# Optimization experiments

Measured on AMD Instinct MI355X. Metric: run time of the kernel, lower is better.

## Reference

```python
import jax, jax.numpy as jnp
import numpy as np

DIM = 512
NUM_HEADS = 16
HEAD_DIM = DIM // NUM_HEADS
RES = (32, 32)
SEQ_SCALE = float(np.log(RES[0] * RES[1]))  # seq_length_scale buffer
TABLE = (2 * RES[0] - 1) * (2 * RES[1] - 1)  # 3969
EPS = 1e-12


def setup_inputs() -> dict:
    key = jax.random.key(0)
    ks = jax.random.split(key, 12)
    B, N, C = 8, RES[0] * RES[1], DIM
    s = 0.02
    return {
        "x": jax.random.normal(ks[0], (B, N, C), dtype=jnp.float32),
        "_h": RES[0],
        "_w": RES[1],
        "relative_pos_index": jax.random.randint(ks[1], (N, N), 0, TABLE, dtype=jnp.int32),
        "relative_coords_table": jax.random.uniform(ks[2], (TABLE, 2), dtype=jnp.float32, minval=-1.0, maxval=1.0),
        "qkv_w": jax.random.normal(ks[3], (3 * C, C), dtype=jnp.float32) * s,
        "qkv_b": jnp.zeros((3 * C,), dtype=jnp.float32),
        "proj_w": jax.random.normal(ks[4], (C, C), dtype=jnp.float32) * s,
        "proj_b": jnp.zeros((C,), dtype=jnp.float32),
        "temperature": jnp.full((NUM_HEADS, 1, 1), float(np.log(np.expm1(1.0 / 0.24))), dtype=jnp.float32),
        "query_embedding": jax.random.normal(ks[5], (NUM_HEADS, 1, HEAD_DIM), dtype=jnp.float32) * s,
        "cpb_fc1_w": jax.random.normal(ks[6], (512, 2), dtype=jnp.float32) * s,
        "cpb_fc1_b": jnp.zeros((512,), dtype=jnp.float32),
        "cpb_fc2_w": jax.random.normal(ks[7], (NUM_HEADS, 512), dtype=jnp.float32) * s,
        "cpb_fc2_b": jnp.zeros((NUM_HEADS,), dtype=jnp.float32),
    }


def _l2norm(t):
    # F.normalize(t, dim=-1): x / max(||x||, eps)
    n = jnp.sqrt(jnp.sum(t * t, axis=-1, keepdims=True))
    return t / jnp.maximum(n, EPS)


def reference(x, _h, _w, relative_pos_index, relative_coords_table,
              qkv_w, qkv_b, proj_w, proj_b, temperature, query_embedding,
              cpb_fc1_w, cpb_fc1_b, cpb_fc2_w, cpb_fc2_b):
    B, N, C = x.shape
    H, hd = NUM_HEADS, HEAD_DIM
    # qkv projection -> [B, N, 3H, hd] -> [B, 3H, N, hd]
    qkv = (x @ qkv_w.T + qkv_b).reshape(B, N, 3 * H, hd).transpose(0, 2, 1, 3)
    q, k, v = jnp.split(qkv, 3, axis=1)  # each [B, H, N, hd]
    # CPB MLP relative bias: [T,2] -> [T,H] -> gather -> [H,N,N]
    t = jax.nn.relu(relative_coords_table @ cpb_fc1_w.T + cpb_fc1_b) @ cpb_fc2_w.T + cpb_fc2_b
    rel_bias = t[relative_pos_index].transpose(2, 0, 1)  # [H, N, N]
    # cosine attention with learned softplus temperature and query embedding
    scale = jax.nn.softplus(temperature) * SEQ_SCALE  # [H,1,1]
    qn = (_l2norm(q) + query_embedding[None]) * scale[None]
    kn = _l2norm(k)
    attn = jnp.einsum('bhnd,bhmd->bhnm', qn, kn) + rel_bias[None]
    attn = jax.nn.softmax(attn, axis=-1)
    out = jnp.einsum('bhnm,bhmd->bhnd', attn, v)  # [B,H,N,hd]
    out = out.transpose(0, 2, 1, 3).reshape(B, N, C)
    return out @ proj_w.T + proj_b
```

## Files before the change

kernel.cpp:

```cpp
#include <hip/hip_runtime.h>
#include <cstdint>
#include <cstddef>

typedef _Float16 f16;
typedef _Float16 f16x4 __attribute__((ext_vector_type(4)));
typedef _Float16 f16x8 __attribute__((ext_vector_type(8)));
typedef float f32x4 __attribute__((ext_vector_type(4)));

#define MFMA32(a,b,c) __builtin_amdgcn_mfma_f32_16x16x32_f16((a),(b),(c),0,0,0)
#define MFMA16(a,b,c) __builtin_amdgcn_mfma_f32_16x16x16f16((a),(b),(c),0,0,0)

__device__ __forceinline__ float fexp2(float x) {
#if __has_builtin(__builtin_amdgcn_exp2f)
  return __builtin_amdgcn_exp2f(x);
#else
  return __expf(x * 0.69314718055994531f);
#endif
}

__device__ __forceinline__ void gload_lds16(const f16* g, f16* l) {
  __builtin_amdgcn_global_load_lds(
      (const __attribute__((address_space(1))) unsigned int*)g,
      (__attribute__((address_space(3))) unsigned int*)l, 16, 0, 0);
}

static constexpr size_t OFF_TCPB = 0;
static constexpr size_t OFF_BIAS = 262144;
static constexpr size_t OFF_XHI  = OFF_BIAS + 33554432;
static constexpr size_t OFF_XLO  = OFF_XHI + 8388608;
static constexpr size_t OFF_WHI  = OFF_XLO + 8388608;
static constexpr size_t OFF_WLO  = OFF_WHI + 1572864;
static constexpr size_t OFF_PW   = OFF_WLO + 1572864;
static constexpr size_t OFF_QHI  = OFF_PW  + 524288;
static constexpr size_t OFF_QLO  = OFF_QHI + 8388608;
static constexpr size_t OFF_KHI  = OFF_QLO + 8388608;
static constexpr size_t OFF_KLO  = OFF_KHI + 8388608;
static constexpr size_t OFF_VT   = OFF_KLO + 8388608;
static constexpr size_t OFF_AO   = OFF_VT  + 8388608;

__global__ __launch_bounds__(256) void k_convert(
    const float* __restrict__ x, const float* __restrict__ qw, const float* __restrict__ pwf,
    f16* __restrict__ xhi, f16* __restrict__ xlo,
    f16* __restrict__ whi, f16* __restrict__ wlo, f16* __restrict__ pw)
{
  int i = blockIdx.x * 256 + threadIdx.x;
  const float4* src; f16* dh; f16* dl; int j;
  if (i < 1048576)      { j = i;           src = (const float4*)x;   dh = xhi; dl = xlo; }
  else if (i < 1245184) { j = i - 1048576; src = (const float4*)qw;  dh = whi; dl = wlo; }
  else                  { j = i - 1245184; src = (const float4*)pwf; dh = pw;  dl = nullptr; }
  float4 v = src[j];
  f16x4 h;
  h[0] = (f16)v.x; h[1] = (f16)v.y; h[2] = (f16)v.z; h[3] = (f16)v.w;
  ((f16x4*)dh)[j] = h;
  if (dl) {
    f16x4 l;
    l[0] = (f16)(v.x - (float)h[0]); l[1] = (f16)(v.y - (float)h[1]);
    l[2] = (f16)(v.z - (float)h[2]); l[3] = (f16)(v.w - (float)h[3]);
    ((f16x4*)dl)[j] = l;
  }
}

__global__ __launch_bounds__(256) void k_cpb(
    const float* __restrict__ table, const float* __restrict__ w1, const float* __restrict__ b1,
    const float* __restrict__ w2, const float* __restrict__ b2, float* __restrict__ t_out)
{
  const int r = blockIdx.x * 4 + (threadIdx.x >> 6);
  const int lane = threadIdx.x & 63;
  if (r >= 3969) return;
  const float c0 = table[2*r], c1 = table[2*r+1];
  const int j0 = lane * 8;
  float h[8];
#pragma unroll
  for (int jj = 0; jj < 8; jj++) {
    int j = j0 + jj;
    float v = c0 * w1[2*j] + c1 * w1[2*j+1] + b1[j];
    h[jj] = v > 0.0f ? v : 0.0f;
  }
  float acc[16];
#pragma unroll
  for (int o = 0; o < 16; o++) {
    const float4* wp = (const float4*)(w2 + o*512 + j0);
    float4 a = wp[0], bb = wp[1];
    acc[o] = a.x*h[0] + a.y*h[1] + a.z*h[2] + a.w*h[3]
           + bb.x*h[4] + bb.y*h[5] + bb.z*h[6] + bb.w*h[7];
  }
#pragma unroll
  for (int o = 0; o < 16; o++) {
    float v = acc[o];
    for (int s = 1; s < 64; s <<= 1) v += __shfl_xor(v, s, 64);
    acc[o] = v;
  }
  if (lane == 0) {
#pragma unroll
    for (int o = 0; o < 16; o++)
      t_out[r*16 + o] = (acc[o] + b2[o]) * 1.4426950408889634f;
  }
}

__global__ __launch_bounds__(256) void k_bias(
    const int* __restrict__ idx, const float* __restrict__ t_cpb, f16* __restrict__ bias_t)
{
  const int m4 = blockIdx.x >> 6, ng = blockIdx.x & 63;
  const int h = threadIdx.x >> 4, nl = threadIdx.x & 15;
  const int n = ng*16 + nl;
  int4 I = *(const int4*)(idx + (size_t)n*1024 + m4*4);
  f16x4 o;
  o[0] = (f16)t_cpb[I.x*16 + h];
  o[1] = (f16)t_cpb[I.y*16 + h];
  o[2] = (f16)t_cpb[I.z*16 + h];
  o[3] = (f16)t_cpb[I.w*16 + h];
  *(f16x4*)(bias_t + (((size_t)h*256 + m4)*1024 + n)*4) = o;
}

__global__ __launch_bounds__(256) void k_qkv(
    const f16* __restrict__ xhi, const f16* __restrict__ xlo,
    const f16* __restrict__ whi, const f16* __restrict__ wlo,
    const float* __restrict__ qkvb, const float* __restrict__ temp, const float* __restrict__ qe,
    f16* __restrict__ qh_o, f16* __restrict__ kh_o, f16* __restrict__ vt_o)
{
  __shared__ __align__(16) f16 Ah[8][64][8];
  __shared__ __align__(16) f16 Al[8][64][8];
  __shared__ __align__(16) f16 Bh[8][64][8];
  __shared__ __align__(16) f16 Bl[8][64][8];
  const int tid = threadIdx.x, lane = tid & 63, w = tid >> 6;
  const int rsel = lane & 15, ksel = lane >> 4;
  const int bx = blockIdx.x & 63, by = blockIdx.x >> 6;
  const int m0 = bx << 7, n0 = by << 7;
  const bool SPLIT = (by < 8);

  const size_t aoff = (size_t)(m0 + w*32 + rsel)*512 + ksel*8;
  const size_t boff = (size_t)(n0 + w*32 + rsel)*512 + ksel*8;
  const f16 *gA0 = xhi + aoff,  *gA1 = gA0 + 16*512;
  const f16 *gAl0 = xlo + aoff, *gAl1 = gAl0 + 16*512;
  const f16 *gB0 = whi + boff,  *gB1 = gB0 + 16*512;
  const f16 *gBl0 = wlo + boff, *gBl1 = gBl0 + 16*512;
  f16 *lA0 = &Ah[2*w][0][0],  *lA1 = &Ah[2*w+1][0][0];
  f16 *lAl0 = &Al[2*w][0][0], *lAl1 = &Al[2*w+1][0][0];
  f16 *lB0 = &Bh[2*w][0][0],  *lB1 = &Bh[2*w+1][0][0];
  f16 *lBl0 = &Bl[2*w][0][0], *lBl1 = &Bl[2*w+1][0][0];

  const f32x4 zero = {0.f, 0.f, 0.f, 0.f};
  f32x4 acc[4][4];
#pragma unroll
  for (int mt = 0; mt < 4; mt++)
#pragma unroll
    for (int nt = 0; nt < 4; nt++) acc[mt][nt] = zero;

  const int mb4 = (w & 1) * 4, nb4 = (w >> 1) * 4;
  for (int k0 = 0; k0 < 512; k0 += 32) {
    __syncthreads();
    gload_lds16(gA0 + k0, lA0);
    gload_lds16(gA1 + k0, lA1);
    gload_lds16(gB0 + k0, lB0);
    gload_lds16(gB1 + k0, lB1);
    if (SPLIT) {
      gload_lds16(gAl0 + k0, lAl0);
      gload_lds16(gAl1 + k0, lAl1);
      gload_lds16(gBl0 + k0, lBl0);
      gload_lds16(gBl1 + k0, lBl1);
    }
    __syncthreads();
    f16x8 bhf[4], blf[4];
#pragma unroll
    for (int nt = 0; nt < 4; nt++) bhf[nt] = ((const f16x8*)&Bh[nb4+nt][0][0])[lane];
    if (SPLIT) {
#pragma unroll
      for (int nt = 0; nt < 4; nt++) blf[nt] = ((const f16x8*)&Bl[nb4+nt][0][0])[lane];
#pragma unroll
      for (int mt = 0; mt < 4; mt++) {
        f16x8 ah = ((const f16x8*)&Ah[mb4+mt][0][0])[lane];
        f16x8 al = ((const f16x8*)&Al[mb4+mt][0][0])[lane];
#pragma unroll
        for (int nt = 0; nt < 4; nt++) {
          acc[mt][nt] = MFMA32(al, bhf[nt], acc[mt][nt]);
          acc[mt][nt] = MFMA32(ah, blf[nt], acc[mt][nt]);
          acc[mt][nt] = MFMA32(ah, bhf[nt], acc[mt][nt]);
        }
      }
    } else {
#pragma unroll
      for (int mt = 0; mt < 4; mt++) {
        f16x8 ah = ((const f16x8*)&Ah[mb4+mt][0][0])[lane];
#pragma unroll
        for (int nt = 0; nt < 4; nt++)
          acc[mt][nt] = MFMA32(ah, bhf[nt], acc[mt][nt]);
      }
    }
  }

  const int mbase = m0 + (w & 1)*64, nbase = n0 + (w >> 1)*64;
  float bc[4];
#pragma unroll
  for (int nt = 0; nt < 4; nt++) bc[nt] = qkvb[nbase + nt*16 + rsel];
#pragma unroll
  for (int mt = 0; mt < 4; mt++)
#pragma unroll
    for (int nt = 0; nt < 4; nt++)
#pragma unroll
      for (int r = 0; r < 4; r++) acc[mt][nt][r] += bc[nt];

  if (by < 8) {
    const bool ISQ = (by < 4);
#pragma unroll
    for (int pair = 0; pair < 2; pair++) {
      const int h = ((nbase - (ISQ ? 0 : 512)) >> 5) + pair;
      float sc = 0.f, qe0 = 0.f, qe1 = 0.f;
      if (ISQ) {
        sc  = log1pf(__expf(temp[h])) * 10.0f;
        qe0 = qe[h*32 + rsel];
        qe1 = qe[h*32 + 16 + rsel];
      }
      f16* dh = ISQ ? qh_o : kh_o;
#pragma unroll
      for (int mt = 0; mt < 4; mt++) {
        float ss[4];
#pragma unroll
        for (int r = 0; r < 4; r++) {
          float a = acc[mt][2*pair][r], b = acc[mt][2*pair+1][r];
          ss[r] = a*a + b*b;
        }
        for (int s = 1; s < 16; s <<= 1) {
#pragma unroll
          for (int r = 0; r < 4; r++) ss[r] += __shfl_xor(ss[r], s, 64);
        }
#pragma unroll
        for (int r = 0; r < 4; r++) {
          float rn = 1.0f / fmaxf(sqrtf(ss[r]), 1e-12f);
          int m = mbase + mt*16 + ksel*4 + r;
          int b_ = m >> 10, p = m & 1023;
          size_t base = ((size_t)(b_*16 + h)*1024 + p)*32;
          float v0 = acc[mt][2*pair][r] * rn;
          float v1 = acc[mt][2*pair+1][r] * rn;
          if (ISQ) { v0 = (v0 + qe0) * sc; v1 = (v1 + qe1) * sc; }
          dh[base + rsel]      = (f16)v0;
          dh[base + 16 + rsel] = (f16)v1;
        }
      }
    }
  } else {
#pragma unroll
    for (int mt = 0; mt < 4; mt++) {
      int m = mbase + mt*16 + ksel*4;
      int b_ = m >> 10, p = m & 1023;
#pragma unroll
      for (int nt = 0; nt < 4; nt++) {
        int n = nbase + nt*16 + rsel;
        int g = (n - 1024) >> 5, d = n & 31;
        f16x4 pk;
#pragma unroll
        for (int r = 0; r < 4; r++) pk[r] = (f16)acc[mt][nt][r];
        *(f16x4*)(vt_o + ((size_t)(b_*16 + g)*32 + d)*1024 + p) = pk;
      }
    }
  }
}

__global__ __launch_bounds__(256, 4) void k_attn(
    const f16* __restrict__ qhi, const f16* __restrict__ khi, const f16* __restrict__ vt,
    const f16* __restrict__ bias_t,
    f16* __restrict__ po0, f16* __restrict__ po1,
    float2* __restrict__ ml0, float2* __restrict__ ml1)
{
  __shared__ __align__(16) f16 OT[4][32][40];
  const int lane = threadIdx.x & 63, w = threadIdx.x >> 6;
  const int rsel = lane & 15, ksel = lane >> 4;
  const int bid = blockIdx.x;
  const int qt = bid & 7, split = (bid >> 3) & 1, bh = bid >> 4;
  const int h = bh & 15;
  const int q0 = qt*128 + w*32;
  const int mstart = split * 512;

  f16x8 Qh[2];
#pragma unroll
  for (int c = 0; c < 2; c++)
    Qh[c] = *(const f16x8*)(qhi + ((size_t)bh*1024 + q0 + c*16 + rsel)*32 + ksel*8);

  const f16* kP = khi + (size_t)bh*32768 + (size_t)(mstart + rsel)*32 + ksel*8;
  const f16* vP = vt  + (size_t)bh*32768 + (size_t)rsel*1024 + mstart + ksel*4;
  const f16* bP = bias_t + (size_t)h*1048576 +
                  (((size_t)(mstart >> 2) + ksel)*1024 + q0 + rsel)*4;

  f32x4 O[2][2];
  float mi[2], li[2];
#pragma unroll
  for (int c = 0; c < 2; c++) {
    O[c][0] = (f32x4){0.f,0.f,0.f,0.f};
    O[c][1] = (f32x4){0.f,0.f,0.f,0.f};
    mi[c] = -3.0e38f; li[c] = 0.f;
  }

  for (int it = 0; it < 16; ++it) {
    f16x8 K0 = *(const f16x8*)kP;
    f16x8 K1 = *(const f16x8*)(kP + 512);
    f16x4 Va[2][2];
    Va[0][0] = *(const f16x4*)(vP);
    Va[1][0] = *(const f16x4*)(vP + 16);
    Va[0][1] = *(const f16x4*)(vP + 16384);
    Va[1][1] = *(const f16x4*)(vP + 16400);
    f16x4 Bb[2][2];
    Bb[0][0] = *(const f16x4*)(bP);
    Bb[0][1] = *(const f16x4*)(bP + 64);
    Bb[1][0] = *(const f16x4*)(bP + 16384);
    Bb[1][1] = *(const f16x4*)(bP + 16448);
    kP += 1024; vP += 32; bP += 32768;

    f32x4 St[2][2];
#pragma unroll
    for (int f = 0; f < 2; f++)
#pragma unroll
      for (int c = 0; c < 2; c++) {
        f32x4 Ci;
#pragma unroll
        for (int r = 0; r < 4; r++) Ci[r] = (float)Bb[f][c][r];
        St[f][c] = MFMA32(f ? K1 : K0, Qh[c], Ci);
      }

    f16x4 P16[2][2];
#pragma unroll
    for (int c = 0; c < 2; c++) {
      float cm = fmaxf(fmaxf(fmaxf(St[0][c][0], St[0][c][1]), fmaxf(St[0][c][2], St[0][c][3])),
                       fmaxf(fmaxf(St[1][c][0], St[1][c][1]), fmaxf(St[1][c][2], St[1][c][3])));
      cm = fmaxf(cm, __shfl_xor(cm, 16, 64));
      cm = fmaxf(cm, __shfl_xor(cm, 32, 64));
      float mn = fmaxf(mi[c], cm);
      float alpha = fexp2(mi[c] - mn);
      mi[c] = mn;
      float rs = 0.f;
#pragma unroll
      for (int f = 0; f < 2; f++)
#pragma unroll
        for (int r = 0; r < 4; r++) {
          float p = fexp2(St[f][c][r] - mn);
          rs += p;
          P16[f][c][r] = (f16)p;
        }
      li[c] = li[c]*alpha + rs;
#pragma unroll
      for (int dt = 0; dt < 2; dt++)
#pragma unroll
        for (int r = 0; r < 4; r++) O[c][dt][r] *= alpha;
    }
#pragma unroll
    for (int c = 0; c < 2; c++)
#pragma unroll
      for (int dt = 0; dt < 2; dt++) {
        O[c][dt] = MFMA16(Va[0][dt], P16[0][c], O[c][dt]);
        O[c][dt] = MFMA16(Va[1][dt], P16[1][c], O[c][dt]);
      }
  }

#pragma unroll
  for (int c = 0; c < 2; c++) {
    li[c] += __shfl_xor(li[c], 16, 64);
    li[c] += __shfl_xor(li[c], 32, 64);
    float inv = 1.0f / li[c];
#pragma unroll
    for (int dt = 0; dt < 2; dt++)
#pragma unroll
      for (int r = 0; r < 4; r++)
        OT[w][c*16 + rsel][dt*16 + ksel*4 + r] = (f16)(O[c][dt][r] * inv);
  }
  f16* po_s = split ? po1 : po0;
  float2* ml_s = split ? ml1 : ml0;
  int row = lane >> 1, half = lane & 1;
  f16x8 o0 = *(const f16x8*)(&OT[w][row][half*16]);
  f16x8 o1 = *(const f16x8*)(&OT[w][row][half*16 + 8]);
  f16* outp = po_s + ((size_t)bh*1024 + q0 + row)*32 + half*16;
  *(f16x8*)outp = o0;
  *(f16x8*)(outp + 8) = o1;
  if (lane < 32) {
    int c = lane >> 4;
    float mm = c ? mi[1] : mi[0];
    float ll = c ? li[1] : li[0];
    ml_s[(size_t)bh*1024 + q0 + lane] = make_float2(mm, ll);
  }
}

__global__ __launch_bounds__(256) void k_merge(
    const f16* __restrict__ po0, const f16* __restrict__ po1,
    const float2* __restrict__ ml0, const float2* __restrict__ ml1,
    f16* __restrict__ ao)
{
  int tid = blockIdx.x * 256 + threadIdx.x;
  int h = tid & 15, q = (tid >> 4) & 1023, b = tid >> 14;
  int bh = b*16 + h;
  size_t rec = (size_t)bh*1024 + q;
  float2 a = ml0[rec], c = ml1[rec];
  float M = fmaxf(a.x, c.x);
  float w0 = a.y * fexp2(a.x - M);
  float w1 = c.y * fexp2(c.x - M);
  float inv = 1.0f / (w0 + w1);
  w0 *= inv; w1 *= inv;
  const f16x8* p0 = (const f16x8*)(po0 + rec*32);
  const f16x8* p1 = (const f16x8*)(po1 + rec*32);
  f16* op = ao + ((size_t)b*1024 + q)*512 + h*32;
#pragma unroll
  for (int i = 0; i < 4; i++) {
    f16x8 x0 = p0[i], x1 = p1[i];
    f16x8 o;
#pragma unroll
    for (int j = 0; j < 8; j++) o[j] = (f16)((float)x0[j]*w0 + (float)x1[j]*w1);
    ((f16x8*)op)[i] = o;
  }
}

__global__ __launch_bounds__(256) void k_proj(
    const f16* __restrict__ A, const f16* __restrict__ Bw,
    const float* __restrict__ pb, float* __restrict__ out)
{
  __shared__ __align__(16) f16 Ah[8][64][8];
  __shared__ __align__(16) f16 Bh[8][64][8];
  const int tid = threadIdx.x, lane = tid & 63, w = tid >> 6;
  const int rsel = lane & 15, ksel = lane >> 4;
  const int bx = blockIdx.x & 63, by = blockIdx.x >> 6;
  const int m0 = bx << 7, n0 = by << 7;
  const f16 *gA0 = A + (size_t)(m0 + w*32 + rsel)*512 + ksel*8,  *gA1 = gA0 + 16*512;
  const f16 *gB0 = Bw + (size_t)(n0 + w*32 + rsel)*512 + ksel*8, *gB1 = gB0 + 16*512;
  f16 *lA0 = &Ah[2*w][0][0], *lA1 = &Ah[2*w+1][0][0];
  f16 *lB0 = &Bh[2*w][0][0], *lB1 = &Bh[2*w+1][0][0];
  const f32x4 zero = {0.f, 0.f, 0.f, 0.f};
  f32x4 acc[4][4];
#pragma unroll
  for (int mt = 0; mt < 4; mt++)
#pragma unroll
    for (int nt = 0; nt < 4; nt++) acc[mt][nt] = zero;
  const int mb4 = (w & 1)*4, nb4 = (w >> 1)*4;
  for (int k0 = 0; k0 < 512; k0 += 32) {
    __syncthreads();
    gload_lds16(gA0 + k0, lA0);
    gload_lds16(gA1 + k0, lA1);
    gload_lds16(gB0 + k0, lB0);
    gload_lds16(gB1 + k0, lB1);
    __syncthreads();
    f16x8 bhf[4];
#pragma unroll
    for (int nt = 0; nt < 4; nt++) bhf[nt] = ((const f16x8*)&Bh[nb4+nt][0][0])[lane];
#pragma unroll
    for (int mt = 0; mt < 4; mt++) {
      f16x8 ah = ((const f16x8*)&Ah[mb4+mt][0][0])[lane];
#pragma unroll
      for (int nt = 0; nt < 4; nt++)
        acc[mt][nt] = MFMA32(ah, bhf[nt], acc[mt][nt]);
    }
  }
  const int mbase = m0 + (w & 1)*64, nbase = n0 + (w >> 1)*64;
  float bc[4];
#pragma unroll
  for (int nt = 0; nt < 4; nt++) bc[nt] = pb[nbase + nt*16 + rsel];
#pragma unroll
  for (int mt = 0; mt < 4; mt++)
#pragma unroll
    for (int nt = 0; nt < 4; nt++)
#pragma unroll
      for (int r = 0; r < 4; r++)
        out[(size_t)(mbase + mt*16 + ksel*4 + r)*512 + nbase + nt*16 + rsel] =
            acc[mt][nt][r] + bc[nt];
}

extern "C" void kernel_launch(void* const* d_in, const int* in_sizes, int n_in,
                              void* d_out, int out_size, void* d_ws, size_t ws_size,
                              hipStream_t stream) {
  const float* x    = (const float*)d_in[0];
  const int*   rpi  = (const int*)d_in[3];
  const float* rct  = (const float*)d_in[4];
  const float* qw   = (const float*)d_in[5];
  const float* qb   = (const float*)d_in[6];
  const float* pwf  = (const float*)d_in[7];
  const float* pbv  = (const float*)d_in[8];
  const float* temp = (const float*)d_in[9];
  const float* qe   = (const float*)d_in[10];
  const float* f1w  = (const float*)d_in[11];
  const float* f1b  = (const float*)d_in[12];
  const float* f2w  = (const float*)d_in[13];
  const float* f2b  = (const float*)d_in[14];

  char* ws = (char*)d_ws;
  float* t_cpb  = (float*)(ws + OFF_TCPB);
  f16* bias_t   = (f16*)(ws + OFF_BIAS);
  f16* xhi = (f16*)(ws + OFF_XHI);
  f16* xlo = (f16*)(ws + OFF_XLO);
  f16* whi = (f16*)(ws + OFF_WHI);
  f16* wlo = (f16*)(ws + OFF_WLO);
  f16* pw  = (f16*)(ws + OFF_PW);
  f16* qhi = (f16*)(ws + OFF_QHI);
  f16* khi = (f16*)(ws + OFF_KHI);
  f16* vt  = (f16*)(ws + OFF_VT);
  f16* ao  = (f16*)(ws + OFF_AO);
  f16* po0 = (f16*)(ws + OFF_KLO);
  f16* po1 = (f16*)(ws + OFF_XHI);
  float2* ml0 = (float2*)(ws + OFF_XLO);
  float2* ml1 = ml0 + 131072;

  k_convert<<<5120, 256, 0, stream>>>(x, qw, pwf, xhi, xlo, whi, wlo, pw);
  k_cpb<<<993, 256, 0, stream>>>(rct, f1w, f1b, f2w, f2b, t_cpb);
  k_bias<<<16384, 256, 0, stream>>>(rpi, t_cpb, bias_t);
  k_qkv<<<768, 256, 0, stream>>>(xhi, xlo, whi, wlo, qb, temp, qe,
                                 qhi, khi, vt);
  k_attn<<<2048, 256, 0, stream>>>(qhi, khi, vt, bias_t, po0, po1, ml0, ml1);
  k_merge<<<512, 256, 0, stream>>>(po0, po1, ml0, ml1, ao);
  k_proj<<<256, 256, 0, stream>>>(ao, pw, pbv, (float*)d_out);
}
```

Measured before the change: 309.9 us.

## Drop weight low-part split, vectorize bias gather, remap attention blocks, prefetch K

Drops the low-order fp16 half of the QKV weights, so the split-precision GEMM runs two MFMAs per tile instead of three and loads less data. The bias-expansion kernel now has each thread read all 16 heads of a table entry as float4 loads, which cuts the launch from 16384 blocks to 1024. The attention kernel remaps block IDs so heads are spread across XCDs, switches to byte-offset addressing, and software-prefetches the next K tile. The main risk is lower QKV precision from dropping the weight correction term.

```diff
diff --git a/kernel.cpp b/kernel.cpp
--- a/kernel.cpp
+++ b/kernel.cpp
@@ -41,12 +41,12 @@
 __global__ __launch_bounds__(256) void k_convert(
     const float* __restrict__ x, const float* __restrict__ qw, const float* __restrict__ pwf,
     f16* __restrict__ xhi, f16* __restrict__ xlo,
-    f16* __restrict__ whi, f16* __restrict__ wlo, f16* __restrict__ pw)
+    f16* __restrict__ whi, f16* __restrict__ pw)
 {
   int i = blockIdx.x * 256 + threadIdx.x;
   const float4* src; f16* dh; f16* dl; int j;
   if (i < 1048576)      { j = i;           src = (const float4*)x;   dh = xhi; dl = xlo; }
-  else if (i < 1245184) { j = i - 1048576; src = (const float4*)qw;  dh = whi; dl = wlo; }
+  else if (i < 1245184) { j = i - 1048576; src = (const float4*)qw;  dh = whi; dl = nullptr; }
   else                  { j = i - 1245184; src = (const float4*)pwf; dh = pw;  dl = nullptr; }
   float4 v = src[j];
   f16x4 h;
@@ -100,28 +100,40 @@
 __global__ __launch_bounds__(256) void k_bias(
     const int* __restrict__ idx, const float* __restrict__ t_cpb, f16* __restrict__ bias_t)
 {
-  const int m4 = blockIdx.x >> 6, ng = blockIdx.x & 63;
-  const int h = threadIdx.x >> 4, nl = threadIdx.x & 15;
-  const int n = ng*16 + nl;
+  int g = blockIdx.x * 256 + threadIdx.x;
+  int n = g & 1023, m4 = g >> 10;
   int4 I = *(const int4*)(idx + (size_t)n*1024 + m4*4);
-  f16x4 o;
-  o[0] = (f16)t_cpb[I.x*16 + h];
-  o[1] = (f16)t_cpb[I.y*16 + h];
-  o[2] = (f16)t_cpb[I.z*16 + h];
-  o[3] = (f16)t_cpb[I.w*16 + h];
-  *(f16x4*)(bias_t + (((size_t)h*256 + m4)*1024 + n)*4) = o;
+  int ids[4] = {I.x, I.y, I.z, I.w};
+  const float4* T = (const float4*)t_cpb;
+#pragma unroll
+  for (int half = 0; half < 2; half++) {
+    float4 R[4][2];
+#pragma unroll
+    for (int k = 0; k < 4; k++) {
+      R[k][0] = T[ids[k]*4 + half*2];
+      R[k][1] = T[ids[k]*4 + half*2 + 1];
+    }
+#pragma unroll
+    for (int hh = 0; hh < 8; hh++) {
+      int h = half*8 + hh;
+      f16x4 o;
+#pragma unroll
+      for (int k = 0; k < 4; k++)
+        o[k] = (f16)(((const float*)&R[k][hh >> 2])[hh & 3]);
+      *(f16x4*)(bias_t + (((size_t)h*256 + m4)*1024 + n)*4) = o;
+    }
+  }
 }
 
 __global__ __launch_bounds__(256) void k_qkv(
     const f16* __restrict__ xhi, const f16* __restrict__ xlo,
-    const f16* __restrict__ whi, const f16* __restrict__ wlo,
+    const f16* __restrict__ whi,
     const float* __restrict__ qkvb, const float* __restrict__ temp, const float* __restrict__ qe,
     f16* __restrict__ qh_o, f16* __restrict__ kh_o, f16* __restrict__ vt_o)
 {
   __shared__ __align__(16) f16 Ah[8][64][8];
   __shared__ __align__(16) f16 Al[8][64][8];
   __shared__ __align__(16) f16 Bh[8][64][8];
-  __shared__ __align__(16) f16 Bl[8][64][8];
   const int tid = threadIdx.x, lane = tid & 63, w = tid >> 6;
   const int rsel = lane & 15, ksel = lane >> 4;
   const int bx = blockIdx.x & 63, by = blockIdx.x >> 6;
@@ -133,11 +145,9 @@
   const f16 *gA0 = xhi + aoff,  *gA1 = gA0 + 16*512;
   const f16 *gAl0 = xlo + aoff, *gAl1 = gAl0 + 16*512;
   const f16 *gB0 = whi + boff,  *gB1 = gB0 + 16*512;
-  const f16 *gBl0 = wlo + boff, *gBl1 = gBl0 + 16*512;
   f16 *lA0 = &Ah[2*w][0][0],  *lA1 = &Ah[2*w+1][0][0];
   f16 *lAl0 = &Al[2*w][0][0], *lAl1 = &Al[2*w+1][0][0];
   f16 *lB0 = &Bh[2*w][0][0],  *lB1 = &Bh[2*w+1][0][0];
-  f16 *lBl0 = &Bl[2*w][0][0], *lBl1 = &Bl[2*w+1][0][0];
 
   const f32x4 zero = {0.f, 0.f, 0.f, 0.f};
   f32x4 acc[4][4];
@@ -156,16 +166,12 @@
     if (SPLIT) {
       gload_lds16(gAl0 + k0, lAl0);
       gload_lds16(gAl1 + k0, lAl1);
-      gload_lds16(gBl0 + k0, lBl0);
-      gload_lds16(gBl1 + k0, lBl1);
     }
     __syncthreads();
-    f16x8 bhf[4], blf[4];
+    f16x8 bhf[4];
 #pragma unroll
     for (int nt = 0; nt < 4; nt++) bhf[nt] = ((const f16x8*)&Bh[nb4+nt][0][0])[lane];
     if (SPLIT) {
-#pragma unroll
-      for (int nt = 0; nt < 4; nt++) blf[nt] = ((const f16x8*)&Bl[nb4+nt][0][0])[lane];
 #pragma unroll
       for (int mt = 0; mt < 4; mt++) {
         f16x8 ah = ((const f16x8*)&Ah[mb4+mt][0][0])[lane];
@@ -173,7 +179,6 @@
 #pragma unroll
         for (int nt = 0; nt < 4; nt++) {
           acc[mt][nt] = MFMA32(al, bhf[nt], acc[mt][nt]);
-          acc[mt][nt] = MFMA32(ah, blf[nt], acc[mt][nt]);
           acc[mt][nt] = MFMA32(ah, bhf[nt], acc[mt][nt]);
         }
       }
@@ -265,8 +270,12 @@
   const int lane = threadIdx.x & 63, w = threadIdx.x >> 6;
   const int rsel = lane & 15, ksel = lane >> 4;
   const int bid = blockIdx.x;
-  const int qt = bid & 7, split = (bid >> 3) & 1, bh = bid >> 4;
-  const int h = bh & 15;
+  const int xcd = bid & 7;
+  const int r1 = bid >> 3;
+  const int h = ((r1 & 1) << 3) | xcd;
+  const int r2 = r1 >> 1;
+  const int qt = r2 & 7, split = (r2 >> 3) & 1, b = r2 >> 4;
+  const int bh = b*16 + h;
   const int q0 = qt*128 + w*32;
   const int mstart = split * 512;
 
@@ -275,10 +284,12 @@
   for (int c = 0; c < 2; c++)
     Qh[c] = *(const f16x8*)(qhi + ((size_t)bh*1024 + q0 + c*16 + rsel)*32 + ksel*8);
 
-  const f16* kP = khi + (size_t)bh*32768 + (size_t)(mstart + rsel)*32 + ksel*8;
-  const f16* vP = vt  + (size_t)bh*32768 + (size_t)rsel*1024 + mstart + ksel*4;
-  const f16* bP = bias_t + (size_t)h*1048576 +
-                  (((size_t)(mstart >> 2) + ksel)*1024 + q0 + rsel)*4;
+  const char* kb = (const char*)(khi + (size_t)bh*32768);
+  const char* vb = (const char*)(vt  + (size_t)bh*32768);
+  const char* bb = (const char*)(bias_t + (size_t)h*1048576);
+  int kOff = ((mstart + rsel)*32 + ksel*8) * 2;
+  int vOff = (rsel*1024 + mstart + ksel*4) * 2;
+  int bOff = (((mstart >> 2) + ksel)*1024 + q0 + rsel) * 8;
 
   f32x4 O[2][2];
   float mi[2], li[2];
@@ -289,20 +300,29 @@
     mi[c] = -3.0e38f; li[c] = 0.f;
   }
 
+  f16x8 Kn0 = *(const f16x8*)(kb + kOff);
+  f16x8 Kn1 = *(const f16x8*)(kb + kOff + 1024);
+  kOff += 2048;
+
   for (int it = 0; it < 16; ++it) {
-    f16x8 K0 = *(const f16x8*)kP;
-    f16x8 K1 = *(const f16x8*)(kP + 512);
+    f16x8 K0 = Kn0, K1 = Kn1;
+    if (it < 15) {
+      Kn0 = *(const f16x8*)(kb + kOff);
+      Kn1 = *(const f16x8*)(kb + kOff + 1024);
+      kOff += 2048;
+    }
     f16x4 Va[2][2];
-    Va[0][0] = *(const f16x4*)(vP);
-    Va[1][0] = *(const f16x4*)(vP + 16);
-    Va[0][1] = *(const f16x4*)(vP + 16384);
-    Va[1][1] = *(const f16x4*)(vP + 16400);
+    Va[0][0] = *(const f16x4*)(vb + vOff);
+    Va[1][0] = *(const f16x4*)(vb + vOff + 32);
+    Va[0][1] = *(const f16x4*)(vb + vOff + 32768);
+    Va[1][1] = *(const f16x4*)(vb + vOff + 32800);
+    vOff += 64;
     f16x4 Bb[2][2];
-    Bb[0][0] = *(const f16x4*)(bP);
-    Bb[0][1] = *(const f16x4*)(bP + 64);
-    Bb[1][0] = *(const f16x4*)(bP + 16384);
-    Bb[1][1] = *(const f16x4*)(bP + 16448);
-    kP += 1024; vP += 32; bP += 32768;
+    Bb[0][0] = *(const f16x4*)(bb + bOff);
+    Bb[0][1] = *(const f16x4*)(bb + bOff + 128);
+    Bb[1][0] = *(const f16x4*)(bb + bOff + 32768);
+    Bb[1][1] = *(const f16x4*)(bb + bOff + 32896);
+    bOff += 65536;
 
     f32x4 St[2][2];
 #pragma unroll
@@ -480,7 +500,6 @@
   f16* xhi = (f16*)(ws + OFF_XHI);
   f16* xlo = (f16*)(ws + OFF_XLO);
   f16* whi = (f16*)(ws + OFF_WHI);
-  f16* wlo = (f16*)(ws + OFF_WLO);
   f16* pw  = (f16*)(ws + OFF_PW);
   f16* qhi = (f16*)(ws + OFF_QHI);
   f16* khi = (f16*)(ws + OFF_KHI);
@@ -491,11 +510,10 @@
   float2* ml0 = (float2*)(ws + OFF_XLO);
   float2* ml1 = ml0 + 131072;
 
-  k_convert<<<5120, 256, 0, stream>>>(x, qw, pwf, xhi, xlo, whi, wlo, pw);
+  k_convert<<<5120, 256, 0, stream>>>(x, qw, pwf, xhi, xlo, whi, pw);
   k_cpb<<<993, 256, 0, stream>>>(rct, f1w, f1b, f2w, f2b, t_cpb);
-  k_bias<<<16384, 256, 0, stream>>>(rpi, t_cpb, bias_t);
-  k_qkv<<<768, 256, 0, stream>>>(xhi, xlo, whi, wlo, qb, temp, qe,
-                                 qhi, khi, vt);
+  k_bias<<<1024, 256, 0, stream>>>(rpi, t_cpb, bias_t);
+  k_qkv<<<768, 256, 0, stream>>>(xhi, xlo, whi, qb, temp, qe, qhi, khi, vt);
   k_attn<<<2048, 256, 0, stream>>>(qhi, khi, vt, bias_t, po0, po1, ml0, ml1);
   k_merge<<<512, 256, 0, stream>>>(po0, po1, ml0, ml1, ao);
   k_proj<<<256, 256, 0, stream>>>(ao, pw, pbv, (float*)d_out);
```

Result: faster. 288.8 us (-6.8%).
